# Kernel optimization log

Hardware: AMD Instinct MI355X
Metric: run time of the kernel (lower is better)

The kernel has to match this reference:

```python
import jax, jax.numpy as jnp
import numpy as np

NUM_EXPERTS = 16
TOP_K = 2
AUX_LOSS_WEIGHT = 0.01


def setup_inputs() -> dict:
    key = jax.random.key(0)
    k1, k2 = jax.random.split(key)
    B, H, W, D = 64, 56, 56, 512
    x = jax.random.normal(k1, (B, H, W, D), dtype=jnp.float32)
    # xavier_uniform for [E, D]
    limit = float(np.sqrt(6.0 / (NUM_EXPERTS + D)))
    expert_queries = jax.random.uniform(k2, (NUM_EXPERTS, D), dtype=jnp.float32,
                                        minval=-limit, maxval=limit)
    temperature = jnp.ones((1,), dtype=jnp.float32)
    return {"x": x, "expert_queries": expert_queries, "temperature": temperature}


def reference(x, expert_queries, temperature):
    # logits: [B, H, W, E]
    logits = jnp.einsum("bhwd,ed->bhwe", x, expert_queries) / temperature[0]
    gate_scores = jax.nn.softmax(logits, axis=-1)
    # aux load-balancing loss (training mode -> top_k)
    avg_gate_scores = gate_scores.mean(axis=(0, 1, 2))  # [E]
    flat = gate_scores.reshape(-1, NUM_EXPERTS)
    _, top_k_idx = jax.lax.top_k(flat, TOP_K)  # [N, k]
    mask = jax.nn.one_hot(top_k_idx, NUM_EXPERTS, dtype=flat.dtype).sum(axis=-2)  # [N, E]
    load = (mask / TOP_K).mean(axis=0)  # [E]
    aux_loss = AUX_LOSS_WEIGHT * (avg_gate_scores * load).mean() * (NUM_EXPERTS ** 2)
    return gate_scores, aux_loss
```

## Files before the change

### kernel.cpp

```cpp
#include <hip/hip_runtime.h>
#include <hip/hip_bf16.h>
#include <math.h>


#define NROWS 200704
#define DDIM 512
#define NEXP 16
#define KSTEPS 16
#define NTILES (NROWS / 16)
#define NBLOCKS 256
#define TPB (NTILES / NBLOCKS)

typedef __attribute__((ext_vector_type(8))) short short8;
typedef __attribute__((ext_vector_type(4))) float f32x4;

static __device__ inline short f2bf(float f) {
    __bf16 h = (__bf16)f;
    return __builtin_bit_cast(short, h);
}

static __device__ inline short8 pack8(float4 a, float4 b) {
    short8 r;
    r[0] = f2bf(a.x); r[1] = f2bf(a.y); r[2] = f2bf(a.z); r[3] = f2bf(a.w);
    r[4] = f2bf(b.x); r[5] = f2bf(b.y); r[6] = f2bf(b.z); r[7] = f2bf(b.w);
    return r;
}

__global__ __launch_bounds__(1024, 4) void gate_kernel(
    const float* __restrict__ x,
    const float* __restrict__ q,
    const float* __restrict__ temp,
    float* __restrict__ out,
    float* __restrict__ ws)
{
    const int lane = threadIdx.x & 63;
    const int fe = lane & 15;
    const int g  = lane >> 4;

    __shared__ short8 qlds[KSTEPS * 64];
    __shared__ int tctr;
    __shared__ float sred[32];
    __shared__ float ldspad[17000];

    {
        const int idx = threadIdx.x;
        const int s = idx >> 6, ln = idx & 63;
        const int qfe = ln & 15, qg = ln >> 4;
        const float* qp = q + qfe * DDIM + s * 32 + qg * 4;
        float4 a = *reinterpret_cast<const float4*>(qp);
        float4 b = *reinterpret_cast<const float4*>(qp + 16);
        qlds[idx] = pack8(a, b);
    }
    if (threadIdx.x == 0) tctr = 0;
    if (threadIdx.x < 32) sred[threadIdx.x] = 0.0f;
    __syncthreads();

    const float invT = 1.0f / temp[0];
    const size_t tbase = (size_t)blockIdx.x * TPB;

    float sS[4] = {0, 0, 0, 0};
    float sC[4] = {0, 0, 0, 0};

    int t;
    if (lane == 0) t = atomicAdd(&tctr, 1);
    t = __shfl(t, 0, 64);

    while (t < TPB) {
        int tn;
        if (lane == 0) tn = atomicAdd(&tctr, 1);
        tn = __shfl(tn, 0, 64);

        const float* xr = x + (tbase + t) * 16 * DDIM + (size_t)fe * DDIM;
        f32x4 acc = {0.0f, 0.0f, 0.0f, 0.0f};
#pragma unroll
        for (int s = 0; s < KSTEPS; ++s) {
            float4 a = *reinterpret_cast<const float4*>(xr + s * 32 + g * 4);
            float4 b = *reinterpret_cast<const float4*>(xr + s * 32 + g * 4 + 16);
            acc = __builtin_amdgcn_mfma_f32_16x16x32_bf16(
                qlds[s * 64 + lane], pack8(a, b), acc, 0, 0, 0);
        }

        const float l0 = acc[0] * invT, l1 = acc[1] * invT;
        const float l2 = acc[2] * invT, l3 = acc[3] * invT;

        float m = fmaxf(fmaxf(l0, l1), fmaxf(l2, l3));
        m = fmaxf(m, __shfl_xor(m, 16, 64));
        m = fmaxf(m, __shfl_xor(m, 32, 64));

        const float p0 = __expf(l0 - m), p1 = __expf(l1 - m);
        const float p2 = __expf(l2 - m), p3 = __expf(l3 - m);
        float s4 = (p0 + p1) + (p2 + p3);
        s4 += __shfl_xor(s4, 16, 64);
        s4 += __shfl_xor(s4, 32, 64);
        const float inv = 1.0f / s4;
        const float g0 = p0 * inv, g1 = p1 * inv, g2 = p2 * inv, g3 = p3 * inv;

        const float NI = -3.4e38f;
        const float M0 = (l0 == m) ? NI : l0, M1 = (l1 == m) ? NI : l1;
        const float M2 = (l2 == m) ? NI : l2, M3 = (l3 == m) ? NI : l3;
        float m2 = fmaxf(fmaxf(M0, M1), fmaxf(M2, M3));
        m2 = fmaxf(m2, __shfl_xor(m2, 16, 64));
        m2 = fmaxf(m2, __shfl_xor(m2, 32, 64));

        sS[0] += g0; sS[1] += g1; sS[2] += g2; sS[3] += g3;
        sC[0] += (l0 >= m2) ? 1.0f : 0.0f;
        sC[1] += (l1 >= m2) ? 1.0f : 0.0f;
        sC[2] += (l2 >= m2) ? 1.0f : 0.0f;
        sC[3] += (l3 >= m2) ? 1.0f : 0.0f;

        float4 o = make_float4(g0, g1, g2, g3);
        *reinterpret_cast<float4*>(
            out + ((tbase + t) * 16 + fe) * NEXP + g * 4) = o;
        t = tn;
    }

#pragma unroll
    for (int r = 0; r < 4; ++r) {
        sS[r] += __shfl_xor(sS[r], 1, 64);
        sS[r] += __shfl_xor(sS[r], 2, 64);
        sS[r] += __shfl_xor(sS[r], 4, 64);
        sS[r] += __shfl_xor(sS[r], 8, 64);
        sC[r] += __shfl_xor(sC[r], 1, 64);
        sC[r] += __shfl_xor(sC[r], 2, 64);
        sC[r] += __shfl_xor(sC[r], 4, 64);
        sC[r] += __shfl_xor(sC[r], 8, 64);
    }

    if (fe == 0) {
#pragma unroll
        for (int r = 0; r < 4; ++r) {
            atomicAdd(&sred[g * 4 + r], sS[r]);
            atomicAdd(&sred[16 + g * 4 + r], sC[r]);
        }
    }
    if (tctr < 0) ldspad[tctr & 16383] = sS[0];
    __syncthreads();
    if (threadIdx.x < 32) atomicAdd(&ws[threadIdx.x], sred[threadIdx.x]);
    if (tctr < 0) ws[33] = ldspad[-tctr & 16383];
}

__global__ void aux_kernel(const float* __restrict__ ws, float* __restrict__ out) {
    if (threadIdx.x == 0 && blockIdx.x == 0) {
        float a = 0.0f;
#pragma unroll
        for (int e = 0; e < NEXP; ++e) a += ws[e] * ws[16 + e];
        const float n = (float)NROWS;
        out[(size_t)NROWS * NEXP] = 0.08f * a / (n * n);
    }
}

extern "C" void kernel_launch(void* const* d_in, const int* in_sizes, int n_in,
                              void* d_out, int out_size, void* d_ws, size_t ws_size,
                              hipStream_t stream) {
    const float* x = (const float*)d_in[0];
    const float* q = (const float*)d_in[1];
    const float* t = (const float*)d_in[2];
    float* out = (float*)d_out;
    float* ws = (float*)d_ws;

    hipMemsetAsync(ws, 0, 32 * sizeof(float), stream);
    gate_kernel<<<NBLOCKS, 1024, 0, stream>>>(x, q, t, out, ws);
    aux_kernel<<<1, 64, 0, stream>>>(ws, out);
}
```

Baseline: 103.7 us.

## Software-pipeline softmax epilogue and fold aux loss into last finishing block

The main loop now delays the softmax, top-2 and store work for each tile by one iteration, so the MFMA loads for the next tile can overlap the previous tile's epilogue. A final epilogue after the loop handles the last tile. The separate aux_kernel launch is removed: a global atomic counter picks the last block, which computes the aux loss after a threadfence. This removes one launch but adds a register-held accumulator and fence/atomic overhead.

```diff
diff --git a/kernel.cpp b/kernel.cpp
--- a/kernel.cpp
+++ b/kernel.cpp
@@ -61,6 +61,9 @@
     float sS[4] = {0, 0, 0, 0};
     float sC[4] = {0, 0, 0, 0};
 
+    f32x4 accp = {0, 0, 0, 0};
+    int tp = -1;
+
     int t;
     if (lane == 0) t = atomicAdd(&tctr, 1);
     t = __shfl(t, 0, 64);
@@ -80,8 +83,49 @@
                 qlds[s * 64 + lane], pack8(a, b), acc, 0, 0, 0);
         }
 
-        const float l0 = acc[0] * invT, l1 = acc[1] * invT;
-        const float l2 = acc[2] * invT, l3 = acc[3] * invT;
+        if (tp >= 0) {
+            const float l0 = accp[0] * invT, l1 = accp[1] * invT;
+            const float l2 = accp[2] * invT, l3 = accp[3] * invT;
+
+            float m = fmaxf(fmaxf(l0, l1), fmaxf(l2, l3));
+            m = fmaxf(m, __shfl_xor(m, 16, 64));
+            m = fmaxf(m, __shfl_xor(m, 32, 64));
+
+            const float p0 = __expf(l0 - m), p1 = __expf(l1 - m);
+            const float p2 = __expf(l2 - m), p3 = __expf(l3 - m);
+            float s4 = (p0 + p1) + (p2 + p3);
+            s4 += __shfl_xor(s4, 16, 64);
+            s4 += __shfl_xor(s4, 32, 64);
+            const float inv = 1.0f / s4;
+            const float g0 = p0 * inv, g1 = p1 * inv;
+            const float g2 = p2 * inv, g3 = p3 * inv;
+
+            const float NI = -3.4e38f;
+            const float M0 = (l0 == m) ? NI : l0, M1 = (l1 == m) ? NI : l1;
+            const float M2 = (l2 == m) ? NI : l2, M3 = (l3 == m) ? NI : l3;
+            float m2 = fmaxf(fmaxf(M0, M1), fmaxf(M2, M3));
+            m2 = fmaxf(m2, __shfl_xor(m2, 16, 64));
+            m2 = fmaxf(m2, __shfl_xor(m2, 32, 64));
+
+            sS[0] += g0; sS[1] += g1; sS[2] += g2; sS[3] += g3;
+            sC[0] += (l0 >= m2) ? 1.0f : 0.0f;
+            sC[1] += (l1 >= m2) ? 1.0f : 0.0f;
+            sC[2] += (l2 >= m2) ? 1.0f : 0.0f;
+            sC[3] += (l3 >= m2) ? 1.0f : 0.0f;
+
+            float4 o = make_float4(g0, g1, g2, g3);
+            *reinterpret_cast<float4*>(
+                out + ((tbase + tp) * 16 + fe) * NEXP + g * 4) = o;
+        }
+
+        accp = acc;
+        tp = t;
+        t = tn;
+    }
+
+    if (tp >= 0) {
+        const float l0 = accp[0] * invT, l1 = accp[1] * invT;
+        const float l2 = accp[2] * invT, l3 = accp[3] * invT;
 
         float m = fmaxf(fmaxf(l0, l1), fmaxf(l2, l3));
         m = fmaxf(m, __shfl_xor(m, 16, 64));
@@ -93,7 +137,8 @@
         s4 += __shfl_xor(s4, 16, 64);
         s4 += __shfl_xor(s4, 32, 64);
         const float inv = 1.0f / s4;
-        const float g0 = p0 * inv, g1 = p1 * inv, g2 = p2 * inv, g3 = p3 * inv;
+        const float g0 = p0 * inv, g1 = p1 * inv;
+        const float g2 = p2 * inv, g3 = p3 * inv;
 
         const float NI = -3.4e38f;
         const float M0 = (l0 == m) ? NI : l0, M1 = (l1 == m) ? NI : l1;
@@ -110,8 +155,7 @@
 
         float4 o = make_float4(g0, g1, g2, g3);
         *reinterpret_cast<float4*>(
-            out + ((tbase + t) * 16 + fe) * NEXP + g * 4) = o;
-        t = tn;
+            out + ((tbase + tp) * 16 + fe) * NEXP + g * 4) = o;
     }
 
 #pragma unroll
@@ -136,16 +180,23 @@
     if (tctr < 0) ldspad[tctr & 16383] = sS[0];
     __syncthreads();
     if (threadIdx.x < 32) atomicAdd(&ws[threadIdx.x], sred[threadIdx.x]);
-    if (tctr < 0) ws[33] = ldspad[-tctr & 16383];
-}
-
-__global__ void aux_kernel(const float* __restrict__ ws, float* __restrict__ out) {
-    if (threadIdx.x == 0 && blockIdx.x == 0) {
-        float a = 0.0f;
-#pragma unroll
-        for (int e = 0; e < NEXP; ++e) a += ws[e] * ws[16 + e];
-        const float n = (float)NROWS;
-        out[(size_t)NROWS * NEXP] = 0.08f * a / (n * n);
+    if (tctr < 0) ws[34] = ldspad[-tctr & 16383];
+
+    __syncthreads();
+    __threadfence();
+    if (threadIdx.x == 0) {
+        if (atomicAdd((int*)ws + 32, 1) == NBLOCKS - 1) {
+            __threadfence();
+            float a = 0.0f;
+#pragma unroll
+            for (int e = 0; e < NEXP; ++e) {
+                const float Se = atomicAdd(&ws[e], 0.0f);
+                const float Ce = atomicAdd(&ws[16 + e], 0.0f);
+                a += Se * Ce;
+            }
+            const float n = (float)NROWS;
+            out[(size_t)NROWS * NEXP] = 0.08f * a / (n * n);
+        }
     }
 }
 
@@ -158,7 +209,6 @@
     float* out = (float*)d_out;
     float* ws = (float*)d_ws;
 
-    hipMemsetAsync(ws, 0, 32 * sizeof(float), stream);
+    hipMemsetAsync(ws, 0, 35 * sizeof(float), stream);
     gate_kernel<<<NBLOCKS, 1024, 0, stream>>>(x, q, t, out, ws);
-    aux_kernel<<<1, 64, 0, stream>>>(ws, out);
-}
+}
```

New measurement: 178.2 us. 71.9% more time.
